# Optimization experiments

Hardware: AMD Instinct MI355X
Metric: run time of the kernel (lower is better)

Reference implementation:

```python
import jax, jax.numpy as jnp
import numpy as np

N = 8192
IN_F = 512
NFEAT = 512
OUT_F = 512


def setup_inputs() -> dict:
    key = jax.random.key(0)
    k1, k2, k3, k4, k5 = jax.random.split(key, 5)
    stdv = 1.0 / np.sqrt(OUT_F)
    return {
        "input": jax.random.normal(k1, (N, IN_F), dtype=jnp.float32),
        "adj": jax.random.uniform(k2, (N, N), dtype=jnp.float32),
        "x": jax.random.normal(k3, (N, NFEAT), dtype=jnp.float32),
        "weight": jax.random.uniform(k4, (IN_F + N + NFEAT, OUT_F), minval=-stdv, maxval=stdv, dtype=jnp.float32),
        "bias": jax.random.uniform(k5, (OUT_F,), minval=-stdv, maxval=stdv, dtype=jnp.float32),
    }


def reference(input, adj, x, weight, bias):
    # support = [adj @ input | adj | x]  -> [n, in_features + n + nfeat]
    support = jnp.concatenate((adj @ input, adj, x), axis=1)
    return support @ weight + bias
```

## Files before the change

kernel.cpp:

```cpp
#include <hip/hip_runtime.h>
#include <hip/hip_bf16.h>

typedef __attribute__((ext_vector_type(4))) float f32x4;
typedef __attribute__((ext_vector_type(8))) short bf16x8;
typedef __attribute__((ext_vector_type(4))) unsigned short u16x4;
typedef __attribute__((ext_vector_type(8))) unsigned short u16x8;

__device__ __forceinline__ unsigned short f2bf(float f) {
    unsigned int u = __builtin_bit_cast(unsigned int, f);
    u += 0x7fffu + ((u >> 16) & 1u);
    return (unsigned short)(u >> 16);
}

#define SWZ(i) ((i) ^ ((((i) >> 6) & 7) << 3))

constexpr int BM = 64, BN = 128, BK = 64;

__global__ void transpose_cvt(const float* __restrict__ src,
                              unsigned short* __restrict__ dst,
                              int rows, int cols) {
    int idx = blockIdx.x * 256 + threadIdx.x;
    int c = idx / rows;
    int r = idx - c * rows;
    dst[idx] = f2bf(src[(size_t)r * cols + c]);
}

template<int EPI>
__global__ __launch_bounds__(512, 4)
void gemm_k(const float* __restrict__ A, long lda,
            const unsigned short* __restrict__ Bt, long ldb,
            int K,
            const float* __restrict__ epi, long lde,
            const float* __restrict__ bias,
            void* __restrict__ Dptr, long ldd) {
    __shared__ unsigned short sA[2][BM * BK];
    __shared__ unsigned short sB[2][BN * BK];

    const int t = threadIdx.x;
    const int l = t & 63;
    const int w = t >> 6;
    const int wm = w >> 2;
    const int wn = w & 3;

    int mt, nt;
    {
        int lin = blockIdx.y * gridDim.x + blockIdx.x;
        if ((gridDim.y & 7) == 0) {
            int xcd = lin & 7;
            int slot = lin >> 3;
            int ppx = gridDim.y >> 3;
            mt = xcd * ppx + slot / gridDim.x;
            nt = slot % gridDim.x;
        } else {
            mt = blockIdx.y; nt = blockIdx.x;
        }
    }
    const long m0 = (long)mt * BM;
    const long n0 = (long)nt * BN;

    f32x4 acc[2][2];
    #pragma unroll
    for (int m = 0; m < 2; ++m)
        #pragma unroll
        for (int n = 0; n < 2; ++n)
            acc[m][n] = {0.f, 0.f, 0.f, 0.f};

    f32x4 avA[2], avB[2];
    u16x8 bvA[2], bvB[2];

    auto load_glb = [&](int kt, f32x4* av, u16x8* bv) {
        const long k0 = (long)kt * BK;
        #pragma unroll
        for (int r = 0; r < 2; ++r) {
            int e = r * 2048 + t * 4;
            int row = e >> 6, k = e & 63;
            av[r] = *reinterpret_cast<const f32x4*>(&A[(m0 + row) * lda + k0 + k]);
        }
        #pragma unroll
        for (int r = 0; r < 2; ++r) {
            int e = r * 4096 + t * 8;
            int col = e >> 6, k = e & 63;
            bv[r] = *reinterpret_cast<const u16x8*>(&Bt[(n0 + col) * ldb + k0 + k]);
        }
    };

    auto write_lds = [&](int buf, const f32x4* av, const u16x8* bv) {
        #pragma unroll
        for (int r = 0; r < 2; ++r) {
            int e = r * 2048 + t * 4;
            u16x4 wv;
            wv[0] = f2bf(av[r][0]);
            wv[1] = f2bf(av[r][1]);
            wv[2] = f2bf(av[r][2]);
            wv[3] = f2bf(av[r][3]);
            *reinterpret_cast<u16x4*>(&sA[buf][SWZ(e)]) = wv;
        }
        #pragma unroll
        for (int r = 0; r < 2; ++r) {
            int e = r * 4096 + t * 8;
            *reinterpret_cast<u16x8*>(&sB[buf][SWZ(e)]) = bv[r];
        }
    };

    auto compute = [&](int buf) {
        #pragma unroll
        for (int kk = 0; kk < BK; kk += 32) {
            bf16x8 af[2], bfr[2];
            const int kb = kk + ((l >> 4) << 3);
            #pragma unroll
            for (int m = 0; m < 2; ++m) {
                int row = wm * 32 + m * 16 + (l & 15);
                int idx = row * 64 + kb;
                af[m] = *reinterpret_cast<const bf16x8*>(&sA[buf][SWZ(idx)]);
            }
            #pragma unroll
            for (int n = 0; n < 2; ++n) {
                int col = wn * 32 + n * 16 + (l & 15);
                int idx = col * 64 + kb;
                bfr[n] = *reinterpret_cast<const bf16x8*>(&sB[buf][SWZ(idx)]);
            }
            #pragma unroll
            for (int m = 0; m < 2; ++m)
                #pragma unroll
                for (int n = 0; n < 2; ++n)
                    acc[m][n] = __builtin_amdgcn_mfma_f32_16x16x32_bf16(
                        af[m], bfr[n], acc[m][n], 0, 0, 0);
        }
    };

    load_glb(0, avA, bvA);
    write_lds(0, avA, bvA);
    load_glb(1, avB, bvB);
    __syncthreads();

    const int nk = K / BK;
    for (int kt = 0; kt < nk; kt += 2) {
        if (kt + 2 < nk) load_glb(kt + 2, avA, bvA);
        compute(0);
        write_lds(1, avB, bvB);
        __syncthreads();
        if (kt + 3 < nk) load_glb(kt + 3, avB, bvB);
        compute(1);
        if (kt + 2 < nk) write_lds(0, avA, bvA);
        __syncthreads();
    }

    const int jrow = (l >> 4) * 4;
    #pragma unroll
    for (int m = 0; m < 2; ++m) {
        const long row = m0 + wm * 32 + m * 16 + jrow;
        #pragma unroll
        for (int n = 0; n < 2; ++n) {
            const long col = n0 + wn * 32 + n * 16 + (l & 15);
            f32x4 v = acc[m][n];
            if constexpr (EPI == 0) {
                u16x4 o;
                #pragma unroll
                for (int j = 0; j < 4; ++j)
                    o[j] = f2bf(v[j] + epi[(row + j) * lde + col]);
                *reinterpret_cast<u16x4*>(&((unsigned short*)Dptr)[col * ldd + row]) = o;
            } else if constexpr (EPI == 1) {
                float b = bias[col];
                #pragma unroll
                for (int j = 0; j < 4; ++j)
                    ((float*)Dptr)[(row + j) * ldd + col] = v[j] + b;
            } else {
                #pragma unroll
                for (int j = 0; j < 4; ++j)
                    ((float*)Dptr)[(row + j) * ldd + col] =
                        v[j] + epi[(row + j) * lde + col];
            }
        }
    }
}

extern "C" void kernel_launch(void* const* d_in, const int* in_sizes, int n_in,
                              void* d_out, int out_size, void* d_ws, size_t ws_size,
                              hipStream_t stream) {
    const float* input  = (const float*)d_in[0];
    const float* adj    = (const float*)d_in[1];
    const float* x      = (const float*)d_in[2];
    const float* weight = (const float*)d_in[3];
    const float* bias   = (const float*)d_in[4];

    const int N = 8192, IN_F = 512, NFEAT = 512, OUT_F = 512;
    float* out = (float*)d_out;

    unsigned short* Tbt = (unsigned short*)d_ws;
    unsigned short* W1t = Tbt + (size_t)OUT_F * N;
    unsigned short* W3t = W1t + (size_t)OUT_F * IN_F;
    float* C0 = (float*)(W3t + (size_t)OUT_F * NFEAT);

    transpose_cvt<<<dim3((IN_F * OUT_F) / 256), dim3(256), 0, stream>>>(
        weight, W1t, IN_F, OUT_F);
    transpose_cvt<<<dim3((NFEAT * OUT_F) / 256), dim3(256), 0, stream>>>(
        weight + (size_t)(IN_F + N) * OUT_F, W3t, NFEAT, OUT_F);

    dim3 grid(OUT_F / BN, N / BM);

    gemm_k<0><<<grid, 512, 0, stream>>>(
        input, (long)IN_F, W1t, (long)IN_F, IN_F,
        weight + (size_t)IN_F * OUT_F, (long)OUT_F, nullptr,
        Tbt, (long)N);

    gemm_k<1><<<grid, 512, 0, stream>>>(
        x, (long)NFEAT, W3t, (long)NFEAT, NFEAT,
        nullptr, 0, bias,
        C0, (long)OUT_F);

    gemm_k<2><<<grid, 512, 0, stream>>>(
        adj, (long)N, Tbt, (long)N, N,
        C0, (long)OUT_F, nullptr,
        out, (long)OUT_F);
}
```

Baseline: 185.6 us.

## Pre-tile B into swizzled blocks and stream them via direct global-to-LDS loads

B operands (transposed weights and intermediate T) are now stored pre-tiled in swizzled 128x64 bf16 blocks, so each K-step tile can be copied straight into LDS with global_load_lds instead of passing through registers. A loads use inline asm, and explicit vmcnt/lgkmcnt waits, raw s_barrier and sched_barriers build a finer double-buffered pipeline. MFMA sections are wrapped in s_setprio. This cuts VGPR traffic and LDS write instructions for B, but relies on hand-counted wait counts and on grid dimensions divisible by 8.

```diff
diff --git a/kernel.cpp b/kernel.cpp
--- a/kernel.cpp
+++ b/kernel.cpp
@@ -20,15 +20,18 @@
                               unsigned short* __restrict__ dst,
                               int rows, int cols) {
     int idx = blockIdx.x * 256 + threadIdx.x;
-    int c = idx / rows;
-    int r = idx - c * rows;
-    dst[idx] = f2bf(src[(size_t)r * cols + c]);
+    int n = idx / rows;
+    int k = idx - n * rows;
+    unsigned short v = f2bf(src[(size_t)k * cols + n]);
+    int ntile = n >> 7, ktile = k >> 6;
+    dst[((size_t)(ntile * (rows >> 6) + ktile)) * 8192 +
+        SWZ((n & 127) * 64 + (k & 63))] = v;
 }
 
 template<int EPI>
 __global__ __launch_bounds__(512, 4)
 void gemm_k(const float* __restrict__ A, long lda,
-            const unsigned short* __restrict__ Bt, long ldb,
+            const unsigned short* __restrict__ Bt,
             int K,
             const float* __restrict__ epi, long lde,
             const float* __restrict__ bias,
@@ -45,18 +48,16 @@
     int mt, nt;
     {
         int lin = blockIdx.y * gridDim.x + blockIdx.x;
-        if ((gridDim.y & 7) == 0) {
-            int xcd = lin & 7;
-            int slot = lin >> 3;
-            int ppx = gridDim.y >> 3;
-            mt = xcd * ppx + slot / gridDim.x;
-            nt = slot % gridDim.x;
-        } else {
-            mt = blockIdx.y; nt = blockIdx.x;
-        }
+        int xcd = lin & 7;
+        int slot = lin >> 3;
+        int ppx = gridDim.y >> 3;
+        mt = xcd * ppx + slot / gridDim.x;
+        nt = slot % gridDim.x;
     }
     const long m0 = (long)mt * BM;
     const long n0 = (long)nt * BN;
+    const int KT = K >> 6;
+    const unsigned short* Bblk = Bt + (size_t)nt * KT * 8192;
 
     f32x4 acc[2][2];
     #pragma unroll
@@ -65,85 +66,107 @@
         for (int n = 0; n < 2; ++n)
             acc[m][n] = {0.f, 0.f, 0.f, 0.f};
 
-    f32x4 avA[2], avB[2];
-    u16x8 bvA[2], bvB[2];
-
-    auto load_glb = [&](int kt, f32x4* av, u16x8* bv) {
-        const long k0 = (long)kt * BK;
+    f32x4 aX0, aX1, aY0, aY1;
+
+    auto gll_B = [&](int kt, int buf) {
+        const unsigned short* src = Bblk + (size_t)kt * 8192 + t * 8;
         #pragma unroll
         for (int r = 0; r < 2; ++r) {
-            int e = r * 2048 + t * 4;
-            int row = e >> 6, k = e & 63;
-            av[r] = *reinterpret_cast<const f32x4*>(&A[(m0 + row) * lda + k0 + k]);
+            __builtin_amdgcn_global_load_lds(
+                (const __attribute__((address_space(1))) void*)(src + r * 4096),
+                (__attribute__((address_space(3))) void*)&sB[buf][r * 4096 + w * 512],
+                16, 0, 0);
         }
-        #pragma unroll
-        for (int r = 0; r < 2; ++r) {
-            int e = r * 4096 + t * 8;
-            int col = e >> 6, k = e & 63;
-            bv[r] = *reinterpret_cast<const u16x8*>(&Bt[(n0 + col) * ldb + k0 + k]);
-        }
-    };
-
-    auto write_lds = [&](int buf, const f32x4* av, const u16x8* bv) {
-        #pragma unroll
-        for (int r = 0; r < 2; ++r) {
-            int e = r * 2048 + t * 4;
-            u16x4 wv;
-            wv[0] = f2bf(av[r][0]);
-            wv[1] = f2bf(av[r][1]);
-            wv[2] = f2bf(av[r][2]);
-            wv[3] = f2bf(av[r][3]);
-            *reinterpret_cast<u16x4*>(&sA[buf][SWZ(e)]) = wv;
-        }
-        #pragma unroll
-        for (int r = 0; r < 2; ++r) {
-            int e = r * 4096 + t * 8;
-            *reinterpret_cast<u16x8*>(&sB[buf][SWZ(e)]) = bv[r];
-        }
+    };
+
+    auto load_A = [&](int kt, f32x4& a0, f32x4& a1) {
+        const float* p0 = &A[(m0 + (t >> 4)) * lda + (long)kt * BK + ((t & 15) << 2)];
+        const float* p1 = p0 + 32 * lda;
+        asm volatile("global_load_dwordx4 %0, %2, off\n\t"
+                     "global_load_dwordx4 %1, %3, off"
+                     : "=&v"(a0), "=&v"(a1)
+                     : "v"(p0), "v"(p1)
+                     : "memory");
+    };
+
+    auto write_A = [&](int buf, const f32x4& a0, const f32x4& a1) {
+        int e0 = t * 4;
+        u16x4 w0 = {f2bf(a0[0]), f2bf(a0[1]), f2bf(a0[2]), f2bf(a0[3])};
+        *reinterpret_cast<u16x4*>(&sA[buf][SWZ(e0)]) = w0;
+        int e1 = 2048 + t * 4;
+        u16x4 w1 = {f2bf(a1[0]), f2bf(a1[1]), f2bf(a1[2]), f2bf(a1[3])};
+        *reinterpret_cast<u16x4*>(&sA[buf][SWZ(e1)]) = w1;
     };
 
     auto compute = [&](int buf) {
         #pragma unroll
-        for (int kk = 0; kk < BK; kk += 32) {
+        for (int kk = 0; kk < 2; ++kk) {
             bf16x8 af[2], bfr[2];
-            const int kb = kk + ((l >> 4) << 3);
+            const int kb = kk * 32 + ((l >> 4) << 3);
             #pragma unroll
             for (int m = 0; m < 2; ++m) {
                 int row = wm * 32 + m * 16 + (l & 15);
-                int idx = row * 64 + kb;
-                af[m] = *reinterpret_cast<const bf16x8*>(&sA[buf][SWZ(idx)]);
+                af[m] = *reinterpret_cast<const bf16x8*>(&sA[buf][SWZ(row * 64 + kb)]);
             }
             #pragma unroll
             for (int n = 0; n < 2; ++n) {
                 int col = wn * 32 + n * 16 + (l & 15);
-                int idx = col * 64 + kb;
-                bfr[n] = *reinterpret_cast<const bf16x8*>(&sB[buf][SWZ(idx)]);
+                bfr[n] = *reinterpret_cast<const bf16x8*>(&sB[buf][SWZ(col * 64 + kb)]);
             }
+            __builtin_amdgcn_s_setprio(1);
             #pragma unroll
             for (int m = 0; m < 2; ++m)
                 #pragma unroll
                 for (int n = 0; n < 2; ++n)
                     acc[m][n] = __builtin_amdgcn_mfma_f32_16x16x32_bf16(
                         af[m], bfr[n], acc[m][n], 0, 0, 0);
+            __builtin_amdgcn_s_setprio(0);
         }
     };
 
-    load_glb(0, avA, bvA);
-    write_lds(0, avA, bvA);
-    load_glb(1, avB, bvB);
-    __syncthreads();
-
-    const int nk = K / BK;
-    for (int kt = 0; kt < nk; kt += 2) {
-        if (kt + 2 < nk) load_glb(kt + 2, avA, bvA);
+    gll_B(0, 0);
+    load_A(0, aX0, aX1);
+    load_A(1, aY0, aY1);
+    asm volatile("s_waitcnt vmcnt(2)" ::: "memory");
+    __builtin_amdgcn_sched_barrier(0);
+    write_A(0, aX0, aX1);
+    asm volatile("s_waitcnt lgkmcnt(0)" ::: "memory");
+    __builtin_amdgcn_s_barrier();
+    __builtin_amdgcn_sched_barrier(0);
+
+    const int nk = K >> 6;
+    for (int p = 0; p + 2 < nk; p += 2) {
+        gll_B(p + 1, 1);
+        load_A(p + 2, aX0, aX1);
         compute(0);
-        write_lds(1, avB, bvB);
-        __syncthreads();
-        if (kt + 3 < nk) load_glb(kt + 3, avB, bvB);
+        asm volatile("s_waitcnt vmcnt(4)" ::: "memory");
+        __builtin_amdgcn_sched_barrier(0);
+        write_A(1, aY0, aY1);
+        asm volatile("s_waitcnt vmcnt(2) lgkmcnt(0)" ::: "memory");
+        __builtin_amdgcn_s_barrier();
+        __builtin_amdgcn_sched_barrier(0);
+
+        gll_B(p + 2, 0);
+        load_A(p + 3, aY0, aY1);
         compute(1);
-        if (kt + 2 < nk) write_lds(0, avA, bvA);
-        __syncthreads();
+        asm volatile("s_waitcnt vmcnt(4)" ::: "memory");
+        __builtin_amdgcn_sched_barrier(0);
+        write_A(0, aX0, aX1);
+        asm volatile("s_waitcnt vmcnt(2) lgkmcnt(0)" ::: "memory");
+        __builtin_amdgcn_s_barrier();
+        __builtin_amdgcn_sched_barrier(0);
     }
+
+    gll_B(nk - 1, 1);
+    compute(0);
+    asm volatile("s_waitcnt vmcnt(2)" ::: "memory");
+    __builtin_amdgcn_sched_barrier(0);
+    write_A(1, aY0, aY1);
+    asm volatile("s_waitcnt vmcnt(0) lgkmcnt(0)" ::: "memory");
+    __builtin_amdgcn_s_barrier();
+    __builtin_amdgcn_sched_barrier(0);
+
+    compute(1);
 
     const int jrow = (l >> 4) * 4;
     #pragma unroll
@@ -158,7 +181,11 @@
                 #pragma unroll
                 for (int j = 0; j < 4; ++j)
                     o[j] = f2bf(v[j] + epi[(row + j) * lde + col]);
-                *reinterpret_cast<u16x4*>(&((unsigned short*)Dptr)[col * ldd + row]) = o;
+                int ntile = (int)(col >> 7), cl = (int)(col & 127);
+                int ktile = (int)(row >> 6), kk = (int)(row & 63);
+                *reinterpret_cast<u16x4*>(
+                    &((unsigned short*)Dptr)[((size_t)(ntile * (int)ldd + ktile)) * 8192 +
+                                             SWZ(cl * 64 + kk)]) = o;
             } else if constexpr (EPI == 1) {
                 float b = bias[col];
                 #pragma unroll
@@ -199,17 +226,17 @@
     dim3 grid(OUT_F / BN, N / BM);
 
     gemm_k<0><<<grid, 512, 0, stream>>>(
-        input, (long)IN_F, W1t, (long)IN_F, IN_F,
+        input, (long)IN_F, W1t, IN_F,
         weight + (size_t)IN_F * OUT_F, (long)OUT_F, nullptr,
-        Tbt, (long)N);
+        Tbt, (long)(N / 64));
 
     gemm_k<1><<<grid, 512, 0, stream>>>(
-        x, (long)NFEAT, W3t, (long)NFEAT, NFEAT,
+        x, (long)NFEAT, W3t, NFEAT,
         nullptr, 0, bias,
         C0, (long)OUT_F);
 
     gemm_k<2><<<grid, 512, 0, stream>>>(
-        adj, (long)N, Tbt, (long)N, N,
+        adj, (long)N, Tbt, N,
         C0, (long)OUT_F, nullptr,
         out, (long)OUT_F);
 }
```

Measured after the change: 186.4 us. Within noise of the previous version (+0.4%).
